# Performance work log

Measured on AMD Instinct MI355X. Metric: run time of the kernel, lower is better.

Reference implementation:

```python
import jax, jax.numpy as jnp
import numpy as np

N, L, H, E = 4, 4096, 8, 64
CHUNK = 128  # chunk size for the blocked causal scan
EPS = 1e-6


def elu_feature_map(x):
    # phi(x) = elu(x) + 1 (default feature map of fast-transformers)
    return jax.nn.elu(x) + 1.0


def causal_dot_product(Q, K, V, chunk=CHUNK):
    """out[n,l,h,:] = sum_{s<=l} (Q[n,l,h,:].K[n,s,h,:]) * V[n,s,h,:].
    Chunked scan over the [E,M] KV state: O(N L H E M) without an [L,L] matrix."""
    n, l, h, e = Q.shape
    m = V.shape[-1]
    nc = l // chunk

    def to_chunks(x):
        # [n, l, h, d] -> [nc, n, h, chunk, d]
        return x.reshape(n, nc, chunk, h, x.shape[-1]).transpose(1, 0, 3, 2, 4)

    q, k, v = to_chunks(Q), to_chunks(K), to_chunks(V)
    tril = jnp.tril(jnp.ones((chunk, chunk), dtype=Q.dtype))

    def step(S, xs):  # S: [n, h, e, m] running sum of k v^T
        qc, kc, vc = xs  # [n, h, chunk, e/m]
        inter = jnp.einsum('nhce,nhem->nhcm', qc, S)
        attn = jnp.einsum('nhce,nhde->nhcd', qc, kc) * tril  # intra-chunk causal
        intra = jnp.einsum('nhcd,nhdm->nhcm', attn, vc)
        S = S + jnp.einsum('nhce,nhcm->nhem', kc, vc)
        return S, inter + intra

    S0 = jnp.zeros((n, h, e, m), dtype=Q.dtype)
    _, out = jax.lax.scan(step, S0, (q, k, v))  # [nc, n, h, chunk, m]
    return out.transpose(1, 0, 3, 2, 4).reshape(n, l, h, m)


def setup_inputs() -> dict:
    key = jax.random.key(0)
    k1, k2, k3 = jax.random.split(key, 3)
    return {
        'queries': jax.random.normal(k1, (N, L, H, E), jnp.float32),
        'keys': jax.random.normal(k2, (N, L, H, E), jnp.float32),
        'values': jax.random.normal(k3, (N, L, H, E), jnp.float32),
        'key_lengths': jnp.ones((N, L), jnp.float32),  # float length mask
    }


def reference(queries, keys, values, key_lengths):
    Q = elu_feature_map(queries)
    K = elu_feature_map(keys) * key_lengths[:, :, None, None]
    # denominator: Z[n,l,h] = 1 / (Q[n,l,h] . cumsum_s<=l K[n,s,h] + eps)
    Z = 1.0 / (jnp.einsum('nlhe,nlhe->nlh', Q, jnp.cumsum(K, axis=1)) + EPS)
    V_new = causal_dot_product(Q, K, values)
    return V_new * Z[:, :, :, None]
```

## Files before the change

kernel.cpp:

```cpp
#include <hip/hip_runtime.h>
#include <math.h>

#define NN 4
#define LL 4096
#define HH 8
#define EE 64
#define CHK 64
#define GSUP 4
#define SUPC (CHK*GSUP)
#define NSUP (LL/SUPC)
#define NH (NN*HH)
#define NBLK (NH*NSUP)
#define NCH64 (LL/CHK)
#define EPSF 1e-6f

typedef float f32x4 __attribute__((ext_vector_type(4)));
typedef __bf16 bf16x8 __attribute__((ext_vector_type(8)));

__device__ __forceinline__ float phi_map(float x) {
  return x > 0.0f ? x + 1.0f : __expf(x);
}

#define MFMA(a, b, c) __builtin_amdgcn_mfma_f32_16x16x32_bf16((a), (b), (c), 0, 0, 0)

__device__ __forceinline__ int swz64(int row, int d) {
  return row * 64 + (d & 7) + 8 * ((d >> 3) ^ ((row >> 2) & 7));
}
__device__ __forceinline__ int frag64(int row, int blk) {
  return row * 64 + 8 * (blk ^ ((row >> 2) & 7));
}

#define K1_ISSUE(J, BUF) { \
  const int l0i = (sc * GSUP + (J)) * CHK; \
  _Pragma("unroll") for (int it = 0; it < 4; ++it) { \
    int f = t + 256 * it; int d = f >> 4; int c4 = (f & 15) << 2; \
    size_t gb = (((size_t)n * LL + (size_t)(l0i + d)) * HH + h) * EE + c4; \
    pk[BUF][it] = *(const float4*)(Kg + gb); \
    pv[BUF][it] = *(const float4*)(Vg + gb); \
    pl[BUF][it] = KLg[n * LL + l0i + d]; } }

#define K1_STAGE(BUF) { \
  _Pragma("unroll") for (int it = 0; it < 4; ++it) { \
    int f = t + 256 * it; int d = f >> 4; int c4 = (f & 15) << 2; \
    float klr = pl[BUF][it]; float4 kk = pk[BUF][it]; float4 vv = pv[BUF][it]; \
    float ka[4] = {phi_map(kk.x) * klr, phi_map(kk.y) * klr, phi_map(kk.z) * klr, phi_map(kk.w) * klr}; \
    float va[4] = {vv.x, vv.y, vv.z, vv.w}; \
    _Pragma("unroll") for (int jj = 0; jj < 4; ++jj) { \
      sKt[BUF][swz64(c4 + jj, d)] = (__bf16)ka[jj]; \
      sVt[BUF][swz64(c4 + jj, d)] = (__bf16)va[jj]; } } }

__global__ __launch_bounds__(256, 2) void k_chunksums(
    const float* __restrict__ Kg, const float* __restrict__ Vg,
    const float* __restrict__ KLg, __bf16* __restrict__ ScG, __bf16* __restrict__ KscG)
{
  __shared__ __bf16 sKt[2][4096];
  __shared__ __bf16 sVt[2][4096];
  const int g = blockIdx.x;
  const int sc = g % NSUP;
  const int nh = g / NSUP;
  const int h = nh % HH;
  const int n = nh / HH;
  const int t = threadIdx.x;
  const int w = t >> 6;
  const int lane = t & 63;
  const int lg = lane >> 4;
  const int li = lane & 15;

  float4 pk[2][4], pv[2][4];
  float pl[2][4];

  K1_ISSUE(0, 0);
  K1_STAGE(0);

  f32x4 acc[4];
  #pragma unroll
  for (int nt = 0; nt < 4; ++nt) acc[nt] = (f32x4){0.f, 0.f, 0.f, 0.f};

  bf16x8 ones;
  #pragma unroll
  for (int i = 0; i < 8; ++i) ones[i] = (__bf16)1.0f;

  #pragma unroll
  for (int j = 0; j < GSUP; ++j) {
    if (j + 1 < GSUP) K1_ISSUE(j + 1, (j + 1) & 1);
    __syncthreads();

    bf16x8 aV0 = *(const bf16x8*)&sVt[j & 1][frag64(16 * w + li, lg)];
    bf16x8 aV1 = *(const bf16x8*)&sVt[j & 1][frag64(16 * w + li, 4 + lg)];

    f32x4 accK[4];
    #pragma unroll
    for (int nt = 0; nt < 4; ++nt) accK[nt] = (f32x4){0.f, 0.f, 0.f, 0.f};

    #pragma unroll
    for (int nt = 0; nt < 4; ++nt) {
      bf16x8 b0 = *(const bf16x8*)&sKt[j & 1][frag64(li + 16 * nt, lg)];
      bf16x8 b1 = *(const bf16x8*)&sKt[j & 1][frag64(li + 16 * nt, 4 + lg)];
      acc[nt] = MFMA(aV0, b0, acc[nt]);
      acc[nt] = MFMA(aV1, b1, acc[nt]);
      if (w == 0) {
        accK[nt] = MFMA(ones, b0, accK[nt]);
        accK[nt] = MFMA(ones, b1, accK[nt]);
      }
    }
    if (w == 0 && lg == 0) {
      #pragma unroll
      for (int nt = 0; nt < 4; ++nt)
        KscG[(size_t)(g * GSUP + j) * 64 + li + 16 * nt] = (__bf16)accK[nt][0];
    }
    if (j + 1 < GSUP) K1_STAGE((j + 1) & 1);
  }

  __bf16* sp = ScG + (size_t)g * 4096;
  #pragma unroll
  for (int nt = 0; nt < 4; ++nt)
    #pragma unroll
    for (int reg = 0; reg < 4; ++reg)
      sp[(16 * w + 4 * lg + reg) * 64 + li + 16 * nt] = (__bf16)acc[nt][reg];
}

__global__ __launch_bounds__(256) void k_prefix(
    __bf16* __restrict__ Sc, __bf16* __restrict__ Ksc)
{
  const int bid = blockIdx.x;
  const int t = threadIdx.x;
  if (bid < NH * 16) {
    const int nh = bid >> 4;
    const int strip = bid & 15;
    const int entry = strip * 256 + t;
    __bf16 v[NSUP];
    #pragma unroll
    for (int c = 0; c < NSUP; ++c)
      v[c] = Sc[((size_t)(nh * NSUP + c) << 12) + entry];
    float run = 0.0f;
    #pragma unroll
    for (int c = 0; c < NSUP; ++c) {
      Sc[((size_t)(nh * NSUP + c) << 12) + entry] = (__bf16)run;
      run += (float)v[c];
    }
  } else {
    const int idx = (bid - NH * 16) * 256 + t;
    const int nh = idx >> 6;
    const int e = idx & 63;
    __bf16 v[NCH64];
    #pragma unroll
    for (int c = 0; c < NCH64; ++c)
      v[c] = Ksc[((size_t)(nh * NCH64 + c) << 6) + e];
    float run = 0.0f;
    #pragma unroll
    for (int c = 0; c < NCH64; ++c) {
      Ksc[((size_t)(nh * NCH64 + c) << 6) + e] = (__bf16)run;
      run += (float)v[c];
    }
  }
}

#define P2_ISSUE(CC, BUF) { \
  const int l0i = (sc * GSUP + (CC)) * CHK; \
  _Pragma("unroll") for (int it = 0; it < 4; ++it) { \
    int f = t + 256 * it; int rr = f >> 4; int c4 = (f & 15) << 2; \
    size_t gb = (((size_t)n * LL + (size_t)(l0i + rr)) * HH + h) * EE + c4; \
    pk[BUF][it] = *(const float4*)(Kg + gb); \
    pv[BUF][it] = *(const float4*)(Vg + gb); \
    pl[BUF][it] = KLg[n * LL + l0i + rr]; } \
  { const float* qrow = Qg + (((size_t)n * LL + (size_t)(l0i + arow)) * HH + h) * EE; \
    pq[BUF][0] = *(const float4*)(qrow + 8 * lg); \
    pq[BUF][1] = *(const float4*)(qrow + 8 * lg + 4); \
    pq[BUF][2] = *(const float4*)(qrow + 32 + 8 * lg); \
    pq[BUF][3] = *(const float4*)(qrow + 32 + 8 * lg + 4); } }

#define P2_STAGE(BUF) { \
  _Pragma("unroll") for (int it = 0; it < 4; ++it) { \
    int f = t + 256 * it; int rr = f >> 4; int c4 = (f & 15) << 2; \
    float klr = pl[BUF][it]; float4 kk = pk[BUF][it]; float4 vv = pv[BUF][it]; \
    float ka[4] = {phi_map(kk.x) * klr, phi_map(kk.y) * klr, phi_map(kk.z) * klr, phi_map(kk.w) * klr}; \
    float va[4] = {vv.x, vv.y, vv.z, vv.w}; \
    __bf16* kd = &sK[BUF][rr][c4]; \
    kd[0] = (__bf16)ka[0]; kd[1] = (__bf16)ka[1]; kd[2] = (__bf16)ka[2]; kd[3] = (__bf16)ka[3]; \
    _Pragma("unroll") for (int jj = 0; jj < 4; ++jj) { \
      sKt[BUF][swz64(c4 + jj, rr)] = (__bf16)ka[jj]; \
      sVt[BUF][swz64(c4 + jj, rr)] = (__bf16)va[jj]; } } }

__global__ __launch_bounds__(256, 2) void k_pass2(
    const float* __restrict__ Qg, const float* __restrict__ Kg,
    const float* __restrict__ Vg, const float* __restrict__ KLg,
    const __bf16* __restrict__ Sp, const __bf16* __restrict__ Ksp,
    float* __restrict__ Og)
{
  __shared__ __bf16 sK[2][64][72];
  __shared__ __bf16 sKt[2][4096];
  __shared__ __bf16 sVt[2][4096];
  __shared__ __bf16 sU[4608];

  const int g = blockIdx.x;
  const int sc = g % NSUP;
  const int nh = g / NSUP;
  const int h = nh % HH;
  const int n = nh / HH;
  const int t = threadIdx.x;
  const int w = t >> 6;
  const int lane = t & 63;
  const int lg = lane >> 4;
  const int li = lane & 15;
  const int arow = 16 * w + li;

  float4 pk[2][4], pv[2][4], pq[2][4];
  float pl[2][4];

  {
    const bf16x8* sp8 = (const bf16x8*)(Sp + (size_t)g * 4096);
    bf16x8 s0 = sp8[2 * t];
    bf16x8 s1 = sp8[2 * t + 1];
    int m = t >> 2;
    int e0 = (t & 3) * 16;
    *(bf16x8*)&sU[m * 72 + e0] = s0;
    *(bf16x8*)&sU[m * 72 + e0 + 8] = s1;
  }

  P2_ISSUE(0, 0);
  P2_STAGE(0);

  float bSp[4][4];
  f32x4 accS[4];
  #pragma unroll
  for (int nt = 0; nt < 4; ++nt) accS[nt] = (f32x4){0.f, 0.f, 0.f, 0.f};

  #pragma unroll
  for (int cc = 0; cc < GSUP; ++cc) {
    __syncthreads();

    if (cc == 0) {
      #pragma unroll
      for (int nt = 0; nt < 4; ++nt)
        #pragma unroll
        for (int reg = 0; reg < 4; ++reg)
          bSp[nt][reg] = (float)sU[(16 * w + 4 * lg + reg) * 72 + 16 * nt + li];
    }

    if (cc + 1 < GSUP) P2_ISSUE(cc + 1, (cc + 1) & 1);

    bf16x8 aQ0, aQ1;
    {
      float4 q0 = pq[cc & 1][0], q1 = pq[cc & 1][1], q2 = pq[cc & 1][2], q3 = pq[cc & 1][3];
      aQ0[0] = (__bf16)phi_map(q0.x); aQ0[1] = (__bf16)phi_map(q0.y);
      aQ0[2] = (__bf16)phi_map(q0.z); aQ0[3] = (__bf16)phi_map(q0.w);
      aQ0[4] = (__bf16)phi_map(q1.x); aQ0[5] = (__bf16)phi_map(q1.y);
      aQ0[6] = (__bf16)phi_map(q1.z); aQ0[7] = (__bf16)phi_map(q1.w);
      aQ1[0] = (__bf16)phi_map(q2.x); aQ1[1] = (__bf16)phi_map(q2.y);
      aQ1[2] = (__bf16)phi_map(q2.z); aQ1[3] = (__bf16)phi_map(q2.w);
      aQ1[4] = (__bf16)phi_map(q3.x); aQ1[5] = (__bf16)phi_map(q3.y);
      aQ1[6] = (__bf16)phi_map(q3.z); aQ1[7] = (__bf16)phi_map(q3.w);
    }

    const __bf16* kb = Ksp + (size_t)(g * GSUP + cc) * 64;
    bf16x8 ks0 = *(const bf16x8*)(kb + 8 * lg);
    bf16x8 ks1 = *(const bf16x8*)(kb + 32 + 8 * lg);

    f32x4 acc[4];
    #pragma unroll
    for (int nt = 0; nt < 4; ++nt) acc[nt] = (f32x4){0.f, 0.f, 0.f, 0.f};
    #pragma unroll
    for (int nt = 0; nt < 4; ++nt) {
      bf16x8 b0 = *(const bf16x8*)&sU[(li + 16 * nt) * 72 + 8 * lg];
      bf16x8 b1 = *(const bf16x8*)&sU[(li + 16 * nt) * 72 + 32 + 8 * lg];
      acc[nt] = MFMA(aQ0, b0, acc[nt]);
      acc[nt] = MFMA(aQ1, b1, acc[nt]);
    }

    float dv = 0.0f;
    #pragma unroll
    for (int i = 0; i < 8; ++i) {
      dv += (float)aQ0[i] * (float)ks0[i];
      dv += (float)aQ1[i] * (float)ks1[i];
    }
    dv += __shfl_xor(dv, 16);
    dv += __shfl_xor(dv, 32);
    float den[4];
    #pragma unroll
    for (int reg = 0; reg < 4; ++reg) den[reg] = __shfl(dv, 4 * lg + reg);

    __syncthreads();

    float rs[4] = {0.f, 0.f, 0.f, 0.f};
    #pragma unroll
    for (int nt = 0; nt < 4; ++nt) {
      f32x4 at2 = (f32x4){0.f, 0.f, 0.f, 0.f};
      if (nt <= w) {
        bf16x8 b0 = *(const bf16x8*)&sK[cc & 1][li + 16 * nt][8 * lg];
        bf16x8 b1 = *(const bf16x8*)&sK[cc & 1][li + 16 * nt][32 + 8 * lg];
        at2 = MFMA(aQ0, b0, at2);
        at2 = MFMA(aQ1, b1, at2);
      }
      #pragma unroll
      for (int reg = 0; reg < 4; ++reg) {
        int row = 16 * w + 4 * lg + reg;
        int col = li + 16 * nt;
        float av = (col <= row) ? at2[reg] : 0.0f;
        rs[reg] += av;
        sU[w * 1152 + (4 * lg + reg) * 72 + col] = (__bf16)av;
      }
    }

    {
      bf16x8 aA0 = *(const bf16x8*)&sU[w * 1152 + li * 72 + 8 * lg];
      bf16x8 aA1 = aA0;
      if (w >= 2) aA1 = *(const bf16x8*)&sU[w * 1152 + li * 72 + 32 + 8 * lg];
      #pragma unroll
      for (int nt = 0; nt < 4; ++nt) {
        bf16x8 bv0 = *(const bf16x8*)&sVt[cc & 1][frag64(li + 16 * nt, lg)];
        acc[nt] = MFMA(aA0, bv0, acc[nt]);
        if (w >= 2) {
          bf16x8 bv1 = *(const bf16x8*)&sVt[cc & 1][frag64(li + 16 * nt, 4 + lg)];
          acc[nt] = MFMA(aA1, bv1, acc[nt]);
        }
      }
    }

    #pragma unroll
    for (int reg = 0; reg < 4; ++reg) {
      float v = rs[reg];
      v += __shfl_xor(v, 1);
      v += __shfl_xor(v, 2);
      v += __shfl_xor(v, 4);
      v += __shfl_xor(v, 8);
      rs[reg] = v;
    }

    const int l0 = (sc * GSUP + cc) * CHK;
    #pragma unroll
    for (int reg = 0; reg < 4; ++reg) {
      float inv = 1.0f / (den[reg] + rs[reg] + EPSF);
      int row = l0 + 16 * w + 4 * lg + reg;
      size_t ob = (((size_t)n * LL + row) * HH + h) * EE + li;
      #pragma unroll
      for (int nt = 0; nt < 4; ++nt)
        Og[ob + 16 * nt] = acc[nt][reg] * inv;
    }

    if (cc + 1 < GSUP) {
      bf16x8 aV0 = *(const bf16x8*)&sVt[cc & 1][frag64(16 * w + li, lg)];
      bf16x8 aV1 = *(const bf16x8*)&sVt[cc & 1][frag64(16 * w + li, 4 + lg)];
      #pragma unroll
      for (int nt = 0; nt < 4; ++nt) {
        bf16x8 b0 = *(const bf16x8*)&sKt[cc & 1][frag64(li + 16 * nt, lg)];
        bf16x8 b1 = *(const bf16x8*)&sKt[cc & 1][frag64(li + 16 * nt, 4 + lg)];
        accS[nt] = MFMA(aV0, b0, accS[nt]);
        accS[nt] = MFMA(aV1, b1, accS[nt]);
      }
      #pragma unroll
      for (int nt = 0; nt < 4; ++nt)
        #pragma unroll
        for (int reg = 0; reg < 4; ++reg)
          sU[(16 * w + 4 * lg + reg) * 72 + 16 * nt + li] =
            (__bf16)(bSp[nt][reg] + accS[nt][reg]);

      P2_STAGE((cc + 1) & 1);
    }
  }
}

extern "C" void kernel_launch(void* const* d_in, const int* in_sizes, int n_in,
                              void* d_out, int out_size, void* d_ws, size_t ws_size,
                              hipStream_t stream) {
  const float* Qg  = (const float*)d_in[0];
  const float* Kg  = (const float*)d_in[1];
  const float* Vg  = (const float*)d_in[2];
  const float* KLg = (const float*)d_in[3];
  float* Og = (float*)d_out;

  __bf16* Sc  = (__bf16*)d_ws;
  __bf16* Ksc = (__bf16*)((char*)d_ws + (size_t)NBLK * 4096 * 2);

  hipLaunchKernelGGL(k_chunksums, dim3(NBLK), dim3(256), 0, stream, Kg, Vg, KLg, Sc, Ksc);
  hipLaunchKernelGGL(k_prefix, dim3(NH * 16 + 8), dim3(256), 0, stream, Sc, Ksc);
  hipLaunchKernelGGL(k_pass2, dim3(NBLK), dim3(256), 0, stream, Qg, Kg, Vg, KLg, Sc, Ksc, Og);
}
```

Baseline: 48.10 us.

## Split pass2 work across eight waves, each owning half the output columns

The pass2 kernel moves from 256 to 512 threads per block. Each row-wave is split into two waves that each compute half of the 64 output and state columns. Row sums are exchanged through a small shared array, and the attention tile gets its own swizzled buffer, which removes one barrier. The phi(Q) conversion moves into the staging step, and the running state is kept in the MFMA accumulators instead of a separate bias array. The aim is more waves per CU to hide latency, at the cost of duplicated Q loads and the denominator dot product per wave pair.

```diff
diff --git a/kernel.cpp b/kernel.cpp
--- a/kernel.cpp
+++ b/kernel.cpp
@@ -157,40 +157,52 @@
 
 #define P2_ISSUE(CC, BUF) { \
   const int l0i = (sc * GSUP + (CC)) * CHK; \
-  _Pragma("unroll") for (int it = 0; it < 4; ++it) { \
-    int f = t + 256 * it; int rr = f >> 4; int c4 = (f & 15) << 2; \
-    size_t gb = (((size_t)n * LL + (size_t)(l0i + rr)) * HH + h) * EE + c4; \
+  _Pragma("unroll") for (int it = 0; it < 2; ++it) { \
+    int f = t + 512 * it; int d = f >> 4; int c4 = (f & 15) << 2; \
+    size_t gb = (((size_t)n * LL + (size_t)(l0i + d)) * HH + h) * EE + c4; \
     pk[BUF][it] = *(const float4*)(Kg + gb); \
     pv[BUF][it] = *(const float4*)(Vg + gb); \
-    pl[BUF][it] = KLg[n * LL + l0i + rr]; } \
-  { const float* qrow = Qg + (((size_t)n * LL + (size_t)(l0i + arow)) * HH + h) * EE; \
-    pq[BUF][0] = *(const float4*)(qrow + 8 * lg); \
-    pq[BUF][1] = *(const float4*)(qrow + 8 * lg + 4); \
-    pq[BUF][2] = *(const float4*)(qrow + 32 + 8 * lg); \
-    pq[BUF][3] = *(const float4*)(qrow + 32 + 8 * lg + 4); } }
+    pl[BUF][it] = KLg[n * LL + l0i + d]; } \
+  { const float* qr = Qg + (((size_t)n * LL + (size_t)(l0i + arow)) * HH + h) * EE; \
+    pq[BUF][0] = *(const float4*)(qr + 8 * lg); \
+    pq[BUF][1] = *(const float4*)(qr + 8 * lg + 4); \
+    pq[BUF][2] = *(const float4*)(qr + 32 + 8 * lg); \
+    pq[BUF][3] = *(const float4*)(qr + 32 + 8 * lg + 4); } }
 
 #define P2_STAGE(BUF) { \
-  _Pragma("unroll") for (int it = 0; it < 4; ++it) { \
-    int f = t + 256 * it; int rr = f >> 4; int c4 = (f & 15) << 2; \
+  _Pragma("unroll") for (int it = 0; it < 2; ++it) { \
+    int f = t + 512 * it; int d = f >> 4; int c4 = (f & 15) << 2; \
     float klr = pl[BUF][it]; float4 kk = pk[BUF][it]; float4 vv = pv[BUF][it]; \
     float ka[4] = {phi_map(kk.x) * klr, phi_map(kk.y) * klr, phi_map(kk.z) * klr, phi_map(kk.w) * klr}; \
     float va[4] = {vv.x, vv.y, vv.z, vv.w}; \
-    __bf16* kd = &sK[BUF][rr][c4]; \
-    kd[0] = (__bf16)ka[0]; kd[1] = (__bf16)ka[1]; kd[2] = (__bf16)ka[2]; kd[3] = (__bf16)ka[3]; \
     _Pragma("unroll") for (int jj = 0; jj < 4; ++jj) { \
-      sKt[BUF][swz64(c4 + jj, rr)] = (__bf16)ka[jj]; \
-      sVt[BUF][swz64(c4 + jj, rr)] = (__bf16)va[jj]; } } }
-
-__global__ __launch_bounds__(256, 2) void k_pass2(
+      sK[BUF][swz64(d, c4 + jj)] = (__bf16)ka[jj]; \
+      sKt[BUF][swz64(c4 + jj, d)] = (__bf16)ka[jj]; \
+      sVt[BUF][swz64(c4 + jj, d)] = (__bf16)va[jj]; } } \
+  { float4 q0 = pq[BUF][0], q1 = pq[BUF][1], q2 = pq[BUF][2], q3 = pq[BUF][3]; \
+    bf16x8 a0, a1; \
+    a0[0] = (__bf16)phi_map(q0.x); a0[1] = (__bf16)phi_map(q0.y); \
+    a0[2] = (__bf16)phi_map(q0.z); a0[3] = (__bf16)phi_map(q0.w); \
+    a0[4] = (__bf16)phi_map(q1.x); a0[5] = (__bf16)phi_map(q1.y); \
+    a0[6] = (__bf16)phi_map(q1.z); a0[7] = (__bf16)phi_map(q1.w); \
+    a1[0] = (__bf16)phi_map(q2.x); a1[1] = (__bf16)phi_map(q2.y); \
+    a1[2] = (__bf16)phi_map(q2.z); a1[3] = (__bf16)phi_map(q2.w); \
+    a1[4] = (__bf16)phi_map(q3.x); a1[5] = (__bf16)phi_map(q3.y); \
+    a1[6] = (__bf16)phi_map(q3.z); a1[7] = (__bf16)phi_map(q3.w); \
+    aQ[BUF][0] = a0; aQ[BUF][1] = a1; } }
+
+__global__ __launch_bounds__(512, 4) void k_pass2(
     const float* __restrict__ Qg, const float* __restrict__ Kg,
     const float* __restrict__ Vg, const float* __restrict__ KLg,
     const __bf16* __restrict__ Sp, const __bf16* __restrict__ Ksp,
     float* __restrict__ Og)
 {
-  __shared__ __bf16 sK[2][64][72];
+  __shared__ __bf16 sK[2][4096];
   __shared__ __bf16 sKt[2][4096];
   __shared__ __bf16 sVt[2][4096];
-  __shared__ __bf16 sU[4608];
+  __shared__ __bf16 sU[4096];
+  __shared__ __bf16 sP[4096];
+  __shared__ float sRS[2][4][16];
 
   const int g = blockIdx.x;
   const int sc = g % NSUP;
@@ -199,74 +211,63 @@
   const int n = nh / HH;
   const int t = threadIdx.x;
   const int w = t >> 6;
+  const int wr = w >> 1;
+  const int wh = w & 1;
   const int lane = t & 63;
   const int lg = lane >> 4;
   const int li = lane & 15;
-  const int arow = 16 * w + li;
-
-  float4 pk[2][4], pv[2][4], pq[2][4];
-  float pl[2][4];
+  const int arow = 16 * wr + li;
+
+  float4 pk[2][2], pv[2][2], pq[2][4];
+  float pl[2][2];
+  bf16x8 aQ[2][2];
 
   {
-    const bf16x8* sp8 = (const bf16x8*)(Sp + (size_t)g * 4096);
-    bf16x8 s0 = sp8[2 * t];
-    bf16x8 s1 = sp8[2 * t + 1];
-    int m = t >> 2;
-    int e0 = (t & 3) * 16;
-    *(bf16x8*)&sU[m * 72 + e0] = s0;
-    *(bf16x8*)&sU[m * 72 + e0 + 8] = s1;
+    bf16x8 s8 = *(const bf16x8*)(Sp + (size_t)g * 4096 + (size_t)t * 8);
+    int m = t >> 3, eb = t & 7;
+    *(bf16x8*)&sU[frag64(m, eb)] = s8;
   }
 
   P2_ISSUE(0, 0);
   P2_STAGE(0);
 
-  float bSp[4][4];
-  f32x4 accS[4];
-  #pragma unroll
-  for (int nt = 0; nt < 4; ++nt) accS[nt] = (f32x4){0.f, 0.f, 0.f, 0.f};
+  f32x4 accS[2];
+  #pragma unroll
+  for (int j = 0; j < 2; ++j) accS[j] = (f32x4){0.f, 0.f, 0.f, 0.f};
 
   #pragma unroll
   for (int cc = 0; cc < GSUP; ++cc) {
+    const int cb = cc & 1, nb = cb ^ 1;
     __syncthreads();
 
     if (cc == 0) {
       #pragma unroll
-      for (int nt = 0; nt < 4; ++nt)
+      for (int j = 0; j < 2; ++j) {
+        const int er = li + 16 * (2 * wh + j);
         #pragma unroll
         for (int reg = 0; reg < 4; ++reg)
-          bSp[nt][reg] = (float)sU[(16 * w + 4 * lg + reg) * 72 + 16 * nt + li];
-    }
-
-    if (cc + 1 < GSUP) P2_ISSUE(cc + 1, (cc + 1) & 1);
-
-    bf16x8 aQ0, aQ1;
-    {
-      float4 q0 = pq[cc & 1][0], q1 = pq[cc & 1][1], q2 = pq[cc & 1][2], q3 = pq[cc & 1][3];
-      aQ0[0] = (__bf16)phi_map(q0.x); aQ0[1] = (__bf16)phi_map(q0.y);
-      aQ0[2] = (__bf16)phi_map(q0.z); aQ0[3] = (__bf16)phi_map(q0.w);
-      aQ0[4] = (__bf16)phi_map(q1.x); aQ0[5] = (__bf16)phi_map(q1.y);
-      aQ0[6] = (__bf16)phi_map(q1.z); aQ0[7] = (__bf16)phi_map(q1.w);
-      aQ1[0] = (__bf16)phi_map(q2.x); aQ1[1] = (__bf16)phi_map(q2.y);
-      aQ1[2] = (__bf16)phi_map(q2.z); aQ1[3] = (__bf16)phi_map(q2.w);
-      aQ1[4] = (__bf16)phi_map(q3.x); aQ1[5] = (__bf16)phi_map(q3.y);
-      aQ1[6] = (__bf16)phi_map(q3.z); aQ1[7] = (__bf16)phi_map(q3.w);
+          accS[j][reg] = (float)sU[swz64(16 * wr + 4 * lg + reg, er)];
+      }
+    }
+
+    if (cc + 1 < GSUP) P2_ISSUE(cc + 1, nb);
+
+    bf16x8 aQ0 = aQ[cb][0], aQ1 = aQ[cb][1];
+
+    f32x4 acc[2];
+    #pragma unroll
+    for (int j = 0; j < 2; ++j) {
+      acc[j] = (f32x4){0.f, 0.f, 0.f, 0.f};
+      const int m = li + 16 * (2 * wh + j);
+      bf16x8 b0 = *(const bf16x8*)&sU[frag64(m, lg)];
+      bf16x8 b1 = *(const bf16x8*)&sU[frag64(m, 4 + lg)];
+      acc[j] = MFMA(aQ0, b0, acc[j]);
+      acc[j] = MFMA(aQ1, b1, acc[j]);
     }
 
     const __bf16* kb = Ksp + (size_t)(g * GSUP + cc) * 64;
     bf16x8 ks0 = *(const bf16x8*)(kb + 8 * lg);
     bf16x8 ks1 = *(const bf16x8*)(kb + 32 + 8 * lg);
-
-    f32x4 acc[4];
-    #pragma unroll
-    for (int nt = 0; nt < 4; ++nt) acc[nt] = (f32x4){0.f, 0.f, 0.f, 0.f};
-    #pragma unroll
-    for (int nt = 0; nt < 4; ++nt) {
-      bf16x8 b0 = *(const bf16x8*)&sU[(li + 16 * nt) * 72 + 8 * lg];
-      bf16x8 b1 = *(const bf16x8*)&sU[(li + 16 * nt) * 72 + 32 + 8 * lg];
-      acc[nt] = MFMA(aQ0, b0, acc[nt]);
-      acc[nt] = MFMA(aQ1, b1, acc[nt]);
-    }
-
     float dv = 0.0f;
     #pragma unroll
     for (int i = 0; i < 8; ++i) {
@@ -279,43 +280,26 @@
     #pragma unroll
     for (int reg = 0; reg < 4; ++reg) den[reg] = __shfl(dv, 4 * lg + reg);
 
-    __syncthreads();
-
     float rs[4] = {0.f, 0.f, 0.f, 0.f};
     #pragma unroll
-    for (int nt = 0; nt < 4; ++nt) {
+    for (int j = 0; j < 2; ++j) {
+      const int ntg = 2 * wh + j;
       f32x4 at2 = (f32x4){0.f, 0.f, 0.f, 0.f};
-      if (nt <= w) {
-        bf16x8 b0 = *(const bf16x8*)&sK[cc & 1][li + 16 * nt][8 * lg];
-        bf16x8 b1 = *(const bf16x8*)&sK[cc & 1][li + 16 * nt][32 + 8 * lg];
+      if (ntg <= wr) {
+        bf16x8 b0 = *(const bf16x8*)&sK[cb][frag64(li + 16 * ntg, lg)];
+        bf16x8 b1 = *(const bf16x8*)&sK[cb][frag64(li + 16 * ntg, 4 + lg)];
         at2 = MFMA(aQ0, b0, at2);
         at2 = MFMA(aQ1, b1, at2);
       }
       #pragma unroll
       for (int reg = 0; reg < 4; ++reg) {
-        int row = 16 * w + 4 * lg + reg;
-        int col = li + 16 * nt;
+        int row = 16 * wr + 4 * lg + reg;
+        int col = li + 16 * ntg;
         float av = (col <= row) ? at2[reg] : 0.0f;
         rs[reg] += av;
-        sU[w * 1152 + (4 * lg + reg) * 72 + col] = (__bf16)av;
-      }
-    }
-
-    {
-      bf16x8 aA0 = *(const bf16x8*)&sU[w * 1152 + li * 72 + 8 * lg];
-      bf16x8 aA1 = aA0;
-      if (w >= 2) aA1 = *(const bf16x8*)&sU[w * 1152 + li * 72 + 32 + 8 * lg];
-      #pragma unroll
-      for (int nt = 0; nt < 4; ++nt) {
-        bf16x8 bv0 = *(const bf16x8*)&sVt[cc & 1][frag64(li + 16 * nt, lg)];
-        acc[nt] = MFMA(aA0, bv0, acc[nt]);
-        if (w >= 2) {
-          bf16x8 bv1 = *(const bf16x8*)&sVt[cc & 1][frag64(li + 16 * nt, 4 + lg)];
-          acc[nt] = MFMA(aA1, bv1, acc[nt]);
-        }
-      }
-    }
-
+        sP[swz64(row, col)] = (__bf16)av;
+      }
+    }
     #pragma unroll
     for (int reg = 0; reg < 4; ++reg) {
       float v = rs[reg];
@@ -325,36 +309,57 @@
       v += __shfl_xor(v, 8);
       rs[reg] = v;
     }
+    if (li == 0) {
+      #pragma unroll
+      for (int reg = 0; reg < 4; ++reg) sRS[wh][wr][4 * lg + reg] = rs[reg];
+    }
+
+    __syncthreads();
+
+    float rsT[4];
+    #pragma unroll
+    for (int reg = 0; reg < 4; ++reg)
+      rsT[reg] = rs[reg] + sRS[wh ^ 1][wr][4 * lg + reg];
+
+    {
+      bf16x8 aP0 = *(const bf16x8*)&sP[frag64(arow, lg)];
+      bf16x8 aP1 = *(const bf16x8*)&sP[frag64(arow, 4 + lg)];
+      #pragma unroll
+      for (int j = 0; j < 2; ++j) {
+        const int m = li + 16 * (2 * wh + j);
+        bf16x8 bv0 = *(const bf16x8*)&sVt[cb][frag64(m, lg)];
+        bf16x8 bv1 = *(const bf16x8*)&sVt[cb][frag64(m, 4 + lg)];
+        acc[j] = MFMA(aP0, bv0, acc[j]);
+        acc[j] = MFMA(aP1, bv1, acc[j]);
+      }
+    }
 
     const int l0 = (sc * GSUP + cc) * CHK;
     #pragma unroll
     for (int reg = 0; reg < 4; ++reg) {
-      float inv = 1.0f / (den[reg] + rs[reg] + EPSF);
-      int row = l0 + 16 * w + 4 * lg + reg;
-      size_t ob = (((size_t)n * LL + row) * HH + h) * EE + li;
-      #pragma unroll
-      for (int nt = 0; nt < 4; ++nt)
-        Og[ob + 16 * nt] = acc[nt][reg] * inv;
+      float inv = 1.0f / (den[reg] + rsT[reg] + EPSF);
+      int row = l0 + 16 * wr + 4 * lg + reg;
+      size_t ob = (((size_t)n * LL + row) * HH + h) * EE;
+      #pragma unroll
+      for (int j = 0; j < 2; ++j)
+        Og[ob + li + 16 * (2 * wh + j)] = acc[j][reg] * inv;
     }
 
     if (cc + 1 < GSUP) {
-      bf16x8 aV0 = *(const bf16x8*)&sVt[cc & 1][frag64(16 * w + li, lg)];
-      bf16x8 aV1 = *(const bf16x8*)&sVt[cc & 1][frag64(16 * w + li, 4 + lg)];
-      #pragma unroll
-      for (int nt = 0; nt < 4; ++nt) {
-        bf16x8 b0 = *(const bf16x8*)&sKt[cc & 1][frag64(li + 16 * nt, lg)];
-        bf16x8 b1 = *(const bf16x8*)&sKt[cc & 1][frag64(li + 16 * nt, 4 + lg)];
-        accS[nt] = MFMA(aV0, b0, accS[nt]);
-        accS[nt] = MFMA(aV1, b1, accS[nt]);
-      }
-      #pragma unroll
-      for (int nt = 0; nt < 4; ++nt)
+      bf16x8 aV0 = *(const bf16x8*)&sVt[cb][frag64(arow, lg)];
+      bf16x8 aV1 = *(const bf16x8*)&sVt[cb][frag64(arow, 4 + lg)];
+      #pragma unroll
+      for (int j = 0; j < 2; ++j) {
+        const int er = li + 16 * (2 * wh + j);
+        bf16x8 bk0 = *(const bf16x8*)&sKt[cb][frag64(er, lg)];
+        bf16x8 bk1 = *(const bf16x8*)&sKt[cb][frag64(er, 4 + lg)];
+        accS[j] = MFMA(aV0, bk0, accS[j]);
+        accS[j] = MFMA(aV1, bk1, accS[j]);
         #pragma unroll
         for (int reg = 0; reg < 4; ++reg)
-          sU[(16 * w + 4 * lg + reg) * 72 + 16 * nt + li] =
-            (__bf16)(bSp[nt][reg] + accS[nt][reg]);
-
-      P2_STAGE((cc + 1) & 1);
+          sU[swz64(16 * wr + 4 * lg + reg, er)] = (__bf16)accS[j][reg];
+      }
+      P2_STAGE(nb);
     }
   }
 }
@@ -373,5 +378,5 @@
 
   hipLaunchKernelGGL(k_chunksums, dim3(NBLK), dim3(256), 0, stream, Kg, Vg, KLg, Sc, Ksc);
   hipLaunchKernelGGL(k_prefix, dim3(NH * 16 + 8), dim3(256), 0, stream, Sc, Ksc);
-  hipLaunchKernelGGL(k_pass2, dim3(NBLK), dim3(256), 0, stream, Qg, Kg, Vg, KLg, Sc, Ksc, Og);
-}
+  hipLaunchKernelGGL(k_pass2, dim3(NBLK), dim3(512), 0, stream, Qg, Kg, Vg, KLg, Sc, Ksc, Og);
+}
```

After: 59.39 us. 23.5% more time.

## Single-buffer pass2 LDS with swizzled state tile and raise occupancy target

Applied to the files above, without the earlier changes.

Drops the double-buffered shared-memory K/V/K^T staging in favour of single buffers, which roughly halves the LDS footprint. The launch bound rises from 2 to 4 blocks per CU. The running state tile in sU moves to a swizzled fragment layout and is reused in place for the masked attention tile. The Q feature map is now computed during staging, and the state accumulator is seeded directly from sU instead of a separate bSp register copy. This cuts register and LDS pressure at the cost of an extra barrier per chunk and less overlap between loading the next chunk and computing the current one.

```diff
diff --git a/kernel.cpp b/kernel.cpp
--- a/kernel.cpp
+++ b/kernel.cpp
@@ -155,42 +155,53 @@
   }
 }
 
-#define P2_ISSUE(CC, BUF) { \
+#define P2_ISSUE(CC) { \
   const int l0i = (sc * GSUP + (CC)) * CHK; \
   _Pragma("unroll") for (int it = 0; it < 4; ++it) { \
-    int f = t + 256 * it; int rr = f >> 4; int c4 = (f & 15) << 2; \
-    size_t gb = (((size_t)n * LL + (size_t)(l0i + rr)) * HH + h) * EE + c4; \
-    pk[BUF][it] = *(const float4*)(Kg + gb); \
-    pv[BUF][it] = *(const float4*)(Vg + gb); \
-    pl[BUF][it] = KLg[n * LL + l0i + rr]; } \
-  { const float* qrow = Qg + (((size_t)n * LL + (size_t)(l0i + arow)) * HH + h) * EE; \
-    pq[BUF][0] = *(const float4*)(qrow + 8 * lg); \
-    pq[BUF][1] = *(const float4*)(qrow + 8 * lg + 4); \
-    pq[BUF][2] = *(const float4*)(qrow + 32 + 8 * lg); \
-    pq[BUF][3] = *(const float4*)(qrow + 32 + 8 * lg + 4); } }
-
-#define P2_STAGE(BUF) { \
+    int f = t + 256 * it; int d = f >> 4; int c4 = (f & 15) << 2; \
+    size_t gb = (((size_t)n * LL + (size_t)(l0i + d)) * HH + h) * EE + c4; \
+    pk[it] = *(const float4*)(Kg + gb); \
+    pv[it] = *(const float4*)(Vg + gb); \
+    pl[it] = KLg[n * LL + l0i + d]; } \
+  { const float* qr = Qg + (((size_t)n * LL + (size_t)(l0i + arow)) * HH + h) * EE; \
+    pq[0] = *(const float4*)(qr + 8 * lg); \
+    pq[1] = *(const float4*)(qr + 8 * lg + 4); \
+    pq[2] = *(const float4*)(qr + 32 + 8 * lg); \
+    pq[3] = *(const float4*)(qr + 32 + 8 * lg + 4); } }
+
+#define P2_STAGE(QB) { \
   _Pragma("unroll") for (int it = 0; it < 4; ++it) { \
-    int f = t + 256 * it; int rr = f >> 4; int c4 = (f & 15) << 2; \
-    float klr = pl[BUF][it]; float4 kk = pk[BUF][it]; float4 vv = pv[BUF][it]; \
+    int f = t + 256 * it; int d = f >> 4; int c4 = (f & 15) << 2; \
+    float klr = pl[it]; float4 kk = pk[it]; float4 vv = pv[it]; \
     float ka[4] = {phi_map(kk.x) * klr, phi_map(kk.y) * klr, phi_map(kk.z) * klr, phi_map(kk.w) * klr}; \
     float va[4] = {vv.x, vv.y, vv.z, vv.w}; \
-    __bf16* kd = &sK[BUF][rr][c4]; \
+    __bf16* kd = &sK[d][c4]; \
     kd[0] = (__bf16)ka[0]; kd[1] = (__bf16)ka[1]; kd[2] = (__bf16)ka[2]; kd[3] = (__bf16)ka[3]; \
     _Pragma("unroll") for (int jj = 0; jj < 4; ++jj) { \
-      sKt[BUF][swz64(c4 + jj, rr)] = (__bf16)ka[jj]; \
-      sVt[BUF][swz64(c4 + jj, rr)] = (__bf16)va[jj]; } } }
-
-__global__ __launch_bounds__(256, 2) void k_pass2(
+      sKt[swz64(c4 + jj, d)] = (__bf16)ka[jj]; \
+      sVt[swz64(c4 + jj, d)] = (__bf16)va[jj]; } } \
+  { float4 q0 = pq[0], q1 = pq[1], q2 = pq[2], q3 = pq[3]; \
+    bf16x8 a0, a1; \
+    a0[0] = (__bf16)phi_map(q0.x); a0[1] = (__bf16)phi_map(q0.y); \
+    a0[2] = (__bf16)phi_map(q0.z); a0[3] = (__bf16)phi_map(q0.w); \
+    a0[4] = (__bf16)phi_map(q1.x); a0[5] = (__bf16)phi_map(q1.y); \
+    a0[6] = (__bf16)phi_map(q1.z); a0[7] = (__bf16)phi_map(q1.w); \
+    a1[0] = (__bf16)phi_map(q2.x); a1[1] = (__bf16)phi_map(q2.y); \
+    a1[2] = (__bf16)phi_map(q2.z); a1[3] = (__bf16)phi_map(q2.w); \
+    a1[4] = (__bf16)phi_map(q3.x); a1[5] = (__bf16)phi_map(q3.y); \
+    a1[6] = (__bf16)phi_map(q3.z); a1[7] = (__bf16)phi_map(q3.w); \
+    aQ[QB][0] = a0; aQ[QB][1] = a1; } }
+
+__global__ __launch_bounds__(256, 4) void k_pass2(
     const float* __restrict__ Qg, const float* __restrict__ Kg,
     const float* __restrict__ Vg, const float* __restrict__ KLg,
     const __bf16* __restrict__ Sp, const __bf16* __restrict__ Ksp,
     float* __restrict__ Og)
 {
-  __shared__ __bf16 sK[2][64][72];
-  __shared__ __bf16 sKt[2][4096];
-  __shared__ __bf16 sVt[2][4096];
-  __shared__ __bf16 sU[4608];
+  __shared__ __bf16 sK[64][72];
+  __shared__ __bf16 sKt[4096];
+  __shared__ __bf16 sVt[4096];
+  __shared__ __bf16 sU[4096];
 
   const int g = blockIdx.x;
   const int sc = g % NSUP;
@@ -204,26 +215,23 @@
   const int li = lane & 15;
   const int arow = 16 * w + li;
 
-  float4 pk[2][4], pv[2][4], pq[2][4];
-  float pl[2][4];
+  float4 pk[4], pv[4], pq[4];
+  float pl[4];
+  bf16x8 aQ[2][2];
 
   {
     const bf16x8* sp8 = (const bf16x8*)(Sp + (size_t)g * 4096);
     bf16x8 s0 = sp8[2 * t];
     bf16x8 s1 = sp8[2 * t + 1];
-    int m = t >> 2;
-    int e0 = (t & 3) * 16;
-    *(bf16x8*)&sU[m * 72 + e0] = s0;
-    *(bf16x8*)&sU[m * 72 + e0 + 8] = s1;
+    int m = t >> 2, eb = (t & 3) * 2;
+    *(bf16x8*)&sU[frag64(m, eb)] = s0;
+    *(bf16x8*)&sU[frag64(m, eb + 1)] = s1;
   }
 
-  P2_ISSUE(0, 0);
+  P2_ISSUE(0);
   P2_STAGE(0);
 
-  float bSp[4][4];
   f32x4 accS[4];
-  #pragma unroll
-  for (int nt = 0; nt < 4; ++nt) accS[nt] = (f32x4){0.f, 0.f, 0.f, 0.f};
 
   #pragma unroll
   for (int cc = 0; cc < GSUP; ++cc) {
@@ -234,39 +242,26 @@
       for (int nt = 0; nt < 4; ++nt)
         #pragma unroll
         for (int reg = 0; reg < 4; ++reg)
-          bSp[nt][reg] = (float)sU[(16 * w + 4 * lg + reg) * 72 + 16 * nt + li];
-    }
-
-    if (cc + 1 < GSUP) P2_ISSUE(cc + 1, (cc + 1) & 1);
-
-    bf16x8 aQ0, aQ1;
-    {
-      float4 q0 = pq[cc & 1][0], q1 = pq[cc & 1][1], q2 = pq[cc & 1][2], q3 = pq[cc & 1][3];
-      aQ0[0] = (__bf16)phi_map(q0.x); aQ0[1] = (__bf16)phi_map(q0.y);
-      aQ0[2] = (__bf16)phi_map(q0.z); aQ0[3] = (__bf16)phi_map(q0.w);
-      aQ0[4] = (__bf16)phi_map(q1.x); aQ0[5] = (__bf16)phi_map(q1.y);
-      aQ0[6] = (__bf16)phi_map(q1.z); aQ0[7] = (__bf16)phi_map(q1.w);
-      aQ1[0] = (__bf16)phi_map(q2.x); aQ1[1] = (__bf16)phi_map(q2.y);
-      aQ1[2] = (__bf16)phi_map(q2.z); aQ1[3] = (__bf16)phi_map(q2.w);
-      aQ1[4] = (__bf16)phi_map(q3.x); aQ1[5] = (__bf16)phi_map(q3.y);
-      aQ1[6] = (__bf16)phi_map(q3.z); aQ1[7] = (__bf16)phi_map(q3.w);
+          accS[nt][reg] = (float)sU[swz64(16 * w + 4 * lg + reg, li + 16 * nt)];
+    }
+
+    if (cc + 1 < GSUP) P2_ISSUE(cc + 1);
+
+    bf16x8 aQ0 = aQ[cc & 1][0], aQ1 = aQ[cc & 1][1];
+
+    f32x4 acc[4];
+    #pragma unroll
+    for (int nt = 0; nt < 4; ++nt) {
+      acc[nt] = (f32x4){0.f, 0.f, 0.f, 0.f};
+      bf16x8 b0 = *(const bf16x8*)&sU[frag64(li + 16 * nt, lg)];
+      bf16x8 b1 = *(const bf16x8*)&sU[frag64(li + 16 * nt, 4 + lg)];
+      acc[nt] = MFMA(aQ0, b0, acc[nt]);
+      acc[nt] = MFMA(aQ1, b1, acc[nt]);
     }
 
     const __bf16* kb = Ksp + (size_t)(g * GSUP + cc) * 64;
     bf16x8 ks0 = *(const bf16x8*)(kb + 8 * lg);
     bf16x8 ks1 = *(const bf16x8*)(kb + 32 + 8 * lg);
-
-    f32x4 acc[4];
-    #pragma unroll
-    for (int nt = 0; nt < 4; ++nt) acc[nt] = (f32x4){0.f, 0.f, 0.f, 0.f};
-    #pragma unroll
-    for (int nt = 0; nt < 4; ++nt) {
-      bf16x8 b0 = *(const bf16x8*)&sU[(li + 16 * nt) * 72 + 8 * lg];
-      bf16x8 b1 = *(const bf16x8*)&sU[(li + 16 * nt) * 72 + 32 + 8 * lg];
-      acc[nt] = MFMA(aQ0, b0, acc[nt]);
-      acc[nt] = MFMA(aQ1, b1, acc[nt]);
-    }
-
     float dv = 0.0f;
     #pragma unroll
     for (int i = 0; i < 8; ++i) {
@@ -286,8 +281,8 @@
     for (int nt = 0; nt < 4; ++nt) {
       f32x4 at2 = (f32x4){0.f, 0.f, 0.f, 0.f};
       if (nt <= w) {
-        bf16x8 b0 = *(const bf16x8*)&sK[cc & 1][li + 16 * nt][8 * lg];
-        bf16x8 b1 = *(const bf16x8*)&sK[cc & 1][li + 16 * nt][32 + 8 * lg];
+        bf16x8 b0 = *(const bf16x8*)&sK[li + 16 * nt][8 * lg];
+        bf16x8 b1 = *(const bf16x8*)&sK[li + 16 * nt][32 + 8 * lg];
         at2 = MFMA(aQ0, b0, at2);
         at2 = MFMA(aQ1, b1, at2);
       }
@@ -297,22 +292,7 @@
         int col = li + 16 * nt;
         float av = (col <= row) ? at2[reg] : 0.0f;
         rs[reg] += av;
-        sU[w * 1152 + (4 * lg + reg) * 72 + col] = (__bf16)av;
-      }
-    }
-
-    {
-      bf16x8 aA0 = *(const bf16x8*)&sU[w * 1152 + li * 72 + 8 * lg];
-      bf16x8 aA1 = aA0;
-      if (w >= 2) aA1 = *(const bf16x8*)&sU[w * 1152 + li * 72 + 32 + 8 * lg];
-      #pragma unroll
-      for (int nt = 0; nt < 4; ++nt) {
-        bf16x8 bv0 = *(const bf16x8*)&sVt[cc & 1][frag64(li + 16 * nt, lg)];
-        acc[nt] = MFMA(aA0, bv0, acc[nt]);
-        if (w >= 2) {
-          bf16x8 bv1 = *(const bf16x8*)&sVt[cc & 1][frag64(li + 16 * nt, 4 + lg)];
-          acc[nt] = MFMA(aA1, bv1, acc[nt]);
-        }
+        sU[swz64(row, col)] = (__bf16)av;
       }
     }
 
@@ -326,6 +306,21 @@
       rs[reg] = v;
     }
 
+    {
+      bf16x8 aP0 = *(const bf16x8*)&sU[frag64(arow, lg)];
+      bf16x8 aP1 = aP0;
+      if (w >= 2) aP1 = *(const bf16x8*)&sU[frag64(arow, 4 + lg)];
+      #pragma unroll
+      for (int nt = 0; nt < 4; ++nt) {
+        bf16x8 bv0 = *(const bf16x8*)&sVt[frag64(li + 16 * nt, lg)];
+        acc[nt] = MFMA(aP0, bv0, acc[nt]);
+        if (w >= 2) {
+          bf16x8 bv1 = *(const bf16x8*)&sVt[frag64(li + 16 * nt, 4 + lg)];
+          acc[nt] = MFMA(aP1, bv1, acc[nt]);
+        }
+      }
+    }
+
     const int l0 = (sc * GSUP + cc) * CHK;
     #pragma unroll
     for (int reg = 0; reg < 4; ++reg) {
@@ -338,22 +333,20 @@
     }
 
     if (cc + 1 < GSUP) {
-      bf16x8 aV0 = *(const bf16x8*)&sVt[cc & 1][frag64(16 * w + li, lg)];
-      bf16x8 aV1 = *(const bf16x8*)&sVt[cc & 1][frag64(16 * w + li, 4 + lg)];
+      bf16x8 aV0 = *(const bf16x8*)&sVt[frag64(arow, lg)];
+      bf16x8 aV1 = *(const bf16x8*)&sVt[frag64(arow, 4 + lg)];
       #pragma unroll
       for (int nt = 0; nt < 4; ++nt) {
-        bf16x8 b0 = *(const bf16x8*)&sKt[cc & 1][frag64(li + 16 * nt, lg)];
-        bf16x8 b1 = *(const bf16x8*)&sKt[cc & 1][frag64(li + 16 * nt, 4 + lg)];
-        accS[nt] = MFMA(aV0, b0, accS[nt]);
-        accS[nt] = MFMA(aV1, b1, accS[nt]);
-      }
-      #pragma unroll
-      for (int nt = 0; nt < 4; ++nt)
+        bf16x8 bk0 = *(const bf16x8*)&sKt[frag64(li + 16 * nt, lg)];
+        bf16x8 bk1 = *(const bf16x8*)&sKt[frag64(li + 16 * nt, 4 + lg)];
+        accS[nt] = MFMA(aV0, bk0, accS[nt]);
+        accS[nt] = MFMA(aV1, bk1, accS[nt]);
         #pragma unroll
         for (int reg = 0; reg < 4; ++reg)
-          sU[(16 * w + 4 * lg + reg) * 72 + 16 * nt + li] =
-            (__bf16)(bSp[nt][reg] + accS[nt][reg]);
-
+          sU[swz64(16 * w + 4 * lg + reg, li + 16 * nt)] = (__bf16)accS[nt][reg];
+      }
+
+      __syncthreads();
       P2_STAGE((cc + 1) & 1);
     }
   }
```

New measurement: 96.87 us. +101.4%, slower.
